# Optimization experiments

Hardware: AMD Instinct MI355X
Metric: run time of the kernel (lower is better)

Reference implementation:

```python
import jax, jax.numpy as jnp
from jax import lax
import numpy as np

EPS = 1e-5
K = 16
NUM_GROUP = 128
D = 384
HEADS = 6
DEPTH = 4
BETA = 0.25

def gelu(x):
    return jax.nn.gelu(x, approximate=False)

def linear(x, w, b):
    return x @ w.T + b

def layer_norm(x, g, b):
    mu = x.mean(-1, keepdims=True)
    var = x.var(-1, keepdims=True)
    return (x - mu) / jnp.sqrt(var + EPS) * g + b

def group_norm(x, gamma, beta, groups):
    B, C = x.shape[0], x.shape[1]
    sp = x.shape[2:]
    xg = x.reshape((B, groups, C // groups) + sp)
    axes = tuple(range(2, xg.ndim))
    mu = xg.mean(axes, keepdims=True)
    var = xg.var(axes, keepdims=True)
    xg = (xg - mu) / jnp.sqrt(var + EPS)
    x = xg.reshape((B, C) + sp)
    shp = (1, C) + (1,) * len(sp)
    return x * gamma.reshape(shp) + beta.reshape(shp)

def knn_idx(q, kp, k):
    # q [B,Nq,3], kp [B,Nk,3] -> idx [B,Nq,k] of k nearest keys
    d = jnp.sum(q * q, -1)[:, :, None] - 2.0 * jnp.einsum('bqd,bkd->bqk', q, kp) + jnp.sum(kp * kp, -1)[:, None, :]
    _, idx = lax.top_k(-d, k)
    return idx

def graph_feature(coor_q, x_q, coor_k, x_k, k):
    # coor [B,3,N], x [B,C,N] -> [B,2C,Nq,k]
    idx = knn_idx(coor_q.transpose(0, 2, 1), coor_k.transpose(0, 2, 1), k)
    feat = jax.vmap(lambda a, i: a[:, i])(x_k, idx)  # [B,C,Nq,k]
    xq = x_q[:, :, :, None]
    return jnp.concatenate([feat - xq, jnp.broadcast_to(xq, feat.shape)], axis=1)

def fps_indices(xyz, m):
    # farthest point sampling, start at index 0 (matches pointnet2)
    B, N, _ = xyz.shape
    def body(carry, _):
        dist, far = carry
        c = jnp.take_along_axis(xyz, far[:, None, None], axis=1)
        d = jnp.sum((xyz - c) ** 2, -1)
        dist = jnp.minimum(dist, d)
        return (dist, jnp.argmax(dist, -1).astype(jnp.int32)), far
    init = (jnp.full((B, N), 1e10, xyz.dtype), jnp.zeros((B,), jnp.int32))
    _, idxs = lax.scan(body, init, None, length=m)
    return idxs.T  # [B,m]

def gather_ch(x, idx):
    return jax.vmap(lambda a, i: a[:, i])(x, idx)

def conv1x1_2d(x, w):
    return jnp.einsum('oc,bcnk->bonk', w, x)

def conv1x1_1d(x, w, b):
    return jnp.einsum('oc,bcn->bon', w, x) + b[None, :, None]

def linear_resize(x, out_len):
    # F.interpolate(mode='linear', align_corners=False) along axis 1 of [B,N,D]
    n = x.shape[1]
    pos = (jnp.arange(out_len, dtype=x.dtype) + 0.5) * (n / out_len) - 0.5
    pos = jnp.clip(pos, 0.0, n - 1.0)
    i0 = jnp.floor(pos).astype(jnp.int32)
    i1 = jnp.minimum(i0 + 1, n - 1)
    w = (pos - i0.astype(x.dtype))[None, :, None]
    return x[:, i0] * (1.0 - w) + x[:, i1] * w

def vq(z, cb, beta):
    d = jnp.sum(z * z, -1, keepdims=True) - 2.0 * (z @ cb.T) + jnp.sum(cb * cb, -1)
    eidx = jnp.argmin(d, -1)
    q = cb[eidx]
    loss = jnp.mean((lax.stop_gradient(z) - q) ** 2) + beta * jnp.mean((z - lax.stop_gradient(q)) ** 2)
    q_st = z + lax.stop_gradient(q - z)  # straight-through
    return q_st, loss, eidx

def forward_core(xyz, it_w, it_b, g1_w, g1_g, g1_bt, g2_w, g2_g, g2_bt, g3_w, g3_g, g3_bt, g4_w, g4_g, g4_bt, pe_w1, pe_b1, pe_w2, pe_b2, ip_w1, ip_b1, ip_w2, ip_b2, ln1_g, ln1_b, qkv_w, qkv_b, o_w, o_b, ln2_g, ln2_b, m1_w, m1_b, m2_w, m2_b, pyr_w1, pyr_b1, pyr_g1, pyr_bt1, pyr_w2, pyr_b2, pyr_g2, pyr_bt2, fus_w, fus_b, cb0, cb1, cb2):
    B = xyz.shape[0]
    x = xyz.transpose(0, 2, 1)  # [B,7,N]
    coor, normal, plane = x[:, :3], x[:, 3:6], x[:, 6:7]
    f = conv1x1_1d(coor, it_w, it_b)  # [B,8,N]

    def edge_conv(cq, fq, ck, fk, w, g, bt, groups):
        h = graph_feature(cq, fq, ck, fk, K)
        h = conv1x1_2d(h, w)
        h = group_norm(h, g, bt, groups)
        h = jnp.where(h > 0, h, 0.2 * h)  # LeakyReLU(0.2)
        return h.max(axis=-1)

    f = edge_conv(coor, f, coor, f, g1_w, g1_g, g1_bt, 4)  # [B,32,N]
    idx = fps_indices(coor.transpose(0, 2, 1), NUM_GROUP)
    coor_q, normal_q, plane_q, f_q = gather_ch(coor, idx), gather_ch(normal, idx), gather_ch(plane, idx), gather_ch(f, idx)
    f = edge_conv(coor_q, f_q, coor, f, g2_w, g2_g, g2_bt, 4)  # [B,64,128]
    coor, normal, plane = coor_q, normal_q, plane_q
    f = edge_conv(coor, f, coor, f, g3_w, g3_g, g3_bt, 4)  # [B,64,128]
    idx = fps_indices(coor.transpose(0, 2, 1), NUM_GROUP)
    coor_q, normal_q, plane_q, f_q = gather_ch(coor, idx), gather_ch(normal, idx), gather_ch(plane, idx), gather_ch(f, idx)
    f = edge_conv(coor_q, f_q, coor, f, g4_w, g4_g, g4_bt, 4)  # [B,128,128]
    coor = coor_q.transpose(0, 2, 1)  # [B,128,3]
    f = f.transpose(0, 2, 1)          # [B,128,128]

    pe = linear(gelu(linear(coor, pe_w1, pe_b1)), pe_w2, pe_b2)
    h = linear(gelu(linear(f, ip_w1, ip_b1)), ip_w2, ip_b2)
    t = h + pe
    hd = D // HEADS
    scale = 1.0 / np.sqrt(hd)
    N = t.shape[1]
    for l in range(DEPTH):
        hn = layer_norm(t, ln1_g[l], ln1_b[l])
        qkv = hn @ qkv_w[l] + qkv_b[l]
        q, k_, v = jnp.split(qkv, 3, axis=-1)
        q = q.reshape(B, N, HEADS, hd)
        k_ = k_.reshape(B, N, HEADS, hd)
        v = v.reshape(B, N, HEADS, hd)
        att = jax.nn.softmax(jnp.einsum('bqhd,bkhd->bhqk', q, k_) * scale, axis=-1)
        o = jnp.einsum('bhqk,bkhd->bqhd', att, v).reshape(B, N, D)
        t = t + o @ o_w[l] + o_b[l]
        hn = layer_norm(t, ln2_g[l], ln2_b[l])
        t = t + gelu(hn @ m1_w[l] + m1_b[l]) @ m2_w[l] + m2_b[l]

    base = t  # [B,128,384]
    cbs = (cb0, cb1, cb2)
    outs, losses, idxs = [], [], []
    prev = None
    for level in range(3):
        res = max(base.shape[1] // (2 ** level), 8)
        if res == base.shape[1]:
            lf = base
        else:
            # adaptive_avg_pool1d with evenly dividing bins == reshape-mean
            lf = base.reshape(B, res, base.shape[1] // res, D).mean(2)
        c = lf.transpose(0, 2, 1)
        c = gelu(group_norm(conv1x1_1d(c, pyr_w1[level], pyr_b1[level]), pyr_g1[level], pyr_bt1[level], 8))
        c = gelu(group_norm(conv1x1_1d(c, pyr_w2[level], pyr_b2[level]), pyr_g2[level], pyr_bt2[level], 8))
        proc = c.transpose(0, 2, 1)
        if level > 0:
            pu = prev if prev.shape[1] == res else linear_resize(prev, res)
            proc = gelu(linear(jnp.concatenate([proc, pu], axis=-1), fus_w[level - 1], fus_b[level - 1]))
        q_st, loss, eidx = vq(proc, cbs[level], BETA)
        outs.append(q_st)
        losses.append(loss)
        idxs.append(eidx)
        prev = q_st
    return outs, losses, idxs

def setup_inputs():
    key = jax.random.key(0)
    cnt = [0]
    def nrm(shape, s=0.02):
        cnt[0] += 1
        return jax.random.normal(jax.random.fold_in(key, cnt[0]), shape, jnp.float32) * s
    L = 4
    inp = {}
    inp['xyz'] = nrm((8, 4096, 7), 1.0)
    inp['it_w'] = nrm((8, 3), 0.3)
    inp['it_b'] = jnp.zeros((8,), jnp.float32)
    inp['g1_w'] = nrm((32, 16), 0.1); inp['g1_g'] = jnp.ones((32,)); inp['g1_bt'] = jnp.zeros((32,))
    inp['g2_w'] = nrm((64, 64), 0.1); inp['g2_g'] = jnp.ones((64,)); inp['g2_bt'] = jnp.zeros((64,))
    inp['g3_w'] = nrm((64, 128), 0.1); inp['g3_g'] = jnp.ones((64,)); inp['g3_bt'] = jnp.zeros((64,))
    inp['g4_w'] = nrm((128, 128), 0.1); inp['g4_g'] = jnp.ones((128,)); inp['g4_bt'] = jnp.zeros((128,))
    inp['pe_w1'] = nrm((128, 3), 0.3); inp['pe_b1'] = jnp.zeros((128,))
    inp['pe_w2'] = nrm((D, 128), 0.05); inp['pe_b2'] = jnp.zeros((D,))
    inp['ip_w1'] = nrm((512, 128), 0.05); inp['ip_b1'] = jnp.zeros((512,))
    inp['ip_w2'] = nrm((D, 512), 0.03); inp['ip_b2'] = jnp.zeros((D,))
    inp['ln1_g'] = jnp.ones((L, D)); inp['ln1_b'] = jnp.zeros((L, D))
    inp['qkv_w'] = nrm((L, D, 3 * D)); inp['qkv_b'] = jnp.zeros((L, 3 * D))
    inp['o_w'] = nrm((L, D, D)); inp['o_b'] = jnp.zeros((L, D))
    inp['ln2_g'] = jnp.ones((L, D)); inp['ln2_b'] = jnp.zeros((L, D))
    inp['m1_w'] = nrm((L, D, 4 * D)); inp['m1_b'] = jnp.zeros((L, 4 * D))
    inp['m2_w'] = nrm((L, 4 * D, D)); inp['m2_b'] = jnp.zeros((L, D))
    inp['pyr_w1'] = nrm((3, 2 * D, D), 0.03); inp['pyr_b1'] = jnp.zeros((3, 2 * D))
    inp['pyr_g1'] = jnp.ones((3, 2 * D)); inp['pyr_bt1'] = jnp.zeros((3, 2 * D))
    inp['pyr_w2'] = nrm((3, D, 2 * D), 0.03); inp['pyr_b2'] = jnp.zeros((3, D))
    inp['pyr_g2'] = jnp.ones((3, D)); inp['pyr_bt2'] = jnp.zeros((3, D))
    inp['fus_w'] = nrm((2, D, 2 * D), 0.03); inp['fus_b'] = jnp.zeros((2, D))
    inp['cb0'] = nrm((8192, D), 0.5)
    inp['cb1'] = nrm((4096, D), 0.5)
    inp['cb2'] = nrm((2048, D), 0.5)
    return inp

def reference(xyz, it_w, it_b, g1_w, g1_g, g1_bt, g2_w, g2_g, g2_bt, g3_w, g3_g, g3_bt, g4_w, g4_g, g4_bt, pe_w1, pe_b1, pe_w2, pe_b2, ip_w1, ip_b1, ip_w2, ip_b2, ln1_g, ln1_b, qkv_w, qkv_b, o_w, o_b, ln2_g, ln2_b, m1_w, m1_b, m2_w, m2_b, pyr_w1, pyr_b1, pyr_g1, pyr_bt1, pyr_w2, pyr_b2, pyr_g2, pyr_bt2, fus_w, fus_b, cb0, cb1, cb2):
    outs, losses, idxs = forward_core(xyz, it_w, it_b, g1_w, g1_g, g1_bt, g2_w, g2_g, g2_bt, g3_w, g3_g, g3_bt, g4_w, g4_g, g4_bt, pe_w1, pe_b1, pe_w2, pe_b2, ip_w1, ip_b1, ip_w2, ip_b2, ln1_g, ln1_b, qkv_w, qkv_b, o_w, o_b, ln2_g, ln2_b, m1_w, m1_b, m2_w, m2_b, pyr_w1, pyr_b1, pyr_g1, pyr_bt1, pyr_w2, pyr_b2, pyr_g2, pyr_bt2, fus_w, fus_b, cb0, cb1, cb2)
    # concat quantized features of the 3 levels (128+64+32 tokens), total VQ loss, per-level indices
    return (jnp.concatenate(outs, axis=1), losses[0] + losses[1] + losses[2], idxs[0], idxs[1], idxs[2])
```

## Files before the change

### kernel.cpp

```cpp
#include <hip/hip_runtime.h>
#include <math.h>

#define EPSF 1e-5f

__device__ __forceinline__ float geluf(float x){
  return 0.5f*x*(1.0f + erff(x*0.70710678118654752440f));
}

typedef __attribute__((ext_vector_type(8))) short bf16x8;
typedef __attribute__((ext_vector_type(4))) float f32x4;

constexpr size_t WQKV = 0;
constexpr size_t WO   = WQKV + (size_t)4*1152*384;
constexpr size_t WM1  = WO   + (size_t)4*384*384;
constexpr size_t WM2  = WM1  + (size_t)4*1536*384;
constexpr size_t WIP1 = WM2  + (size_t)4*384*1536;
constexpr size_t WIP2 = WIP1 + (size_t)512*128;
constexpr size_t WPE2 = WIP2 + (size_t)384*512;
constexpr size_t WPY1 = WPE2 + (size_t)384*128;
constexpr size_t WPY2 = WPY1 + (size_t)3*768*384;
constexpr size_t WFUS = WPY2 + (size_t)3*384*768;
constexpr size_t WTOT = WFUS + (size_t)2*384*768;

__device__ __forceinline__ void split_rne(float x, short& h, short& l){
// ... 55 lines not shown
__global__ void gather_rows(const float* __restrict__ src, const int* __restrict__ idx,
                            float* __restrict__ dst, int B, int C, int N, int M){
  int i = blockIdx.x*blockDim.x + threadIdx.x;
  if(i >= B*M*C) return;
  int c = i % C; int m = (i/C)%M; int b = i/(C*M);
  dst[i] = src[((size_t)b*N + idx[b*M+m])*C + c];
}

__global__ void split_planes(const float* __restrict__ src, short* __restrict__ hi,
                             short* __restrict__ lo, int n4){
  int i = blockIdx.x*blockDim.x + threadIdx.x;
  if(i >= n4) return;
  split_quad(src + (size_t)i*4, (unsigned*)hi, (unsigned*)lo, i);
}

__global__ void split_cb3(const float* __restrict__ c0, const float* __restrict__ c1,
                          const float* __restrict__ c2, short* __restrict__ hi, short* __restrict__ lo){
  constexpr int N1 = 8192*384/4, N2 = 4096*384/4, N3 = 2048*384/4;
  int i = blockIdx.x*blockDim.x + threadIdx.x;
  if(i >= N1+N2+N3) return;
  const float* src; size_t q;
  if(i < N1){ src = c0; q = i; }
  else if(i < N1+N2){ src = c1; q = i - N1; }
  else { src = c2; q = i - N1 - N2; }
  split_quad(src + q*4, (unsigned*)hi, (unsigned*)lo, (size_t)i);
}

__global__ void cbsq3(const float* __restrict__ c0, const float* __restrict__ c1,
                      const float* __restrict__ c2, float* __restrict__ out){
  int c = blockIdx.x*blockDim.x + threadIdx.x;
  if(c >= 14336) return;
  const float* p;
  if(c < 8192) p = c0 + (size_t)c*384;
  else if(c < 12288) p = c1 + (size_t)(c-8192)*384;
  else p = c2 + (size_t)(c-12288)*384;
  float s=0.f;
  for(int d=0;d<384;d++) s = fmaf(p[d],p[d],s);
  out[c] = s;
}

__global__ void split_multi(const float* __restrict__ ip1, const float* __restrict__ ip2,
                            const float* __restrict__ pe2, const float* __restrict__ py1,
                            const float* __restrict__ py2, const float* __restrict__ fus,
                            short* __restrict__ hi, short* __restrict__ lo){
  constexpr int N1 = 512*128/4, N2 = 384*512/4, N3 = 384*128/4;
  constexpr int N4 = 3*768*384/4, N5 = 3*384*768/4, N6 = 2*384*768/4;
  int i = blockIdx.x*blockDim.x + threadIdx.x;
  const float* src; size_t q, dq;
  if(i < N1){ src=ip1; q=i; dq=WIP1/4+q; }
  else if(i < N1+N2){ src=ip2; q=i-N1; dq=WIP2/4+q; }
  else if(i < N1+N2+N3){ src=pe2; q=i-N1-N2; dq=WPE2/4+q; }
  else if(i < N1+N2+N3+N4){ src=py1; q=i-N1-N2-N3; dq=WPY1/4+q; }
  else if(i < N1+N2+N3+N4+N5){ src=py2; q=i-N1-N2-N3-N4; dq=WPY2/4+q; }
  else if(i < N1+N2+N3+N4+N5+N6){ src=fus; q=i-N1-N2-N3-N4-N5; dq=WFUS/4+q; }
  else return;
  split_quad(src + q*4, (unsigned*)hi, (unsigned*)lo, dq);
}

__global__ __launch_bounds__(256) void transpose_split(const float* __restrict__ src,
    short* __restrict__ hi, short* __restrict__ lo, int K, int N,
    size_t sstride, size_t dstride){
  __shared__ float tile[32][33];
  int l = blockIdx.z;
  src += (size_t)l*sstride; hi += (size_t)l*dstride; lo += (size_t)l*dstride;
  int bn = blockIdx.x*32, bk = blockIdx.y*32;
  int tx = threadIdx.x & 31, ty = threadIdx.x >> 5;
  #pragma unroll
  for(int i=ty; i<32; i+=8){
    int k = bk+i, n = bn+tx;
    tile[i][tx] = (k<K && n<N) ? src[(size_t)k*N+n] : 0.f;
  }
  __syncthreads();
  #pragma unroll
  for(int i=ty; i<32; i+=8){
    int n = bn+i, k = bk+tx;
    if(n<N && k<K){
      short h,l2; split_rne(tile[tx][i], h, l2);
      hi[(size_t)n*K+k] = h; lo[(size_t)n*K+k] = l2;
    }
  }
}

#define KNN_K 16
template<int NKMAX, int NT>
__global__ __launch_bounds__(NT) void knn2q_kernel(const float* __restrict__ Q, const float* __restrict__ Kp,
                                                   int* __restrict__ idxout, int B, int Nq, int Nk){
  constexpr int NW = NT/64;
  __shared__ float4 sk[NKMAX];
  __shared__ float scd[NW][2][64];
  __shared__ int   sci[NW][2][64];
  __shared__ int   scnt[NW][2];
  int qb = blockIdx.x*(NW*2);
  int b = qb / Nq;
  const float* kb = Kp + (size_t)b*3*Nk;
  if(threadIdx.x < NW*2) ((int*)scnt)[threadIdx.x] = 0;
  for(int n=threadIdx.x; n<Nk; n+=NT){
    float x = kb[n], y = kb[Nk+n], z = kb[2*Nk+n];
    sk[n] = make_float4(x, y, z, fmaf(x,x, fmaf(y,y, z*z)));
  }
  __syncthreads();
  int wave = threadIdx.x >> 6;
  int lane = threadIdx.x & 63;
  int nq0 = qb + wave*2 - b*Nq;
  float q0x = -2.0f*Q[((size_t)b*3+0)*Nq + nq0];
  float q0y = -2.0f*Q[((size_t)b*3+1)*Nq + nq0];
  float q0z = -2.0f*Q[((size_t)b*3+2)*Nq + nq0];
  float q1x = -2.0f*Q[((size_t)b*3+0)*Nq + nq0+1];
  float q1y = -2.0f*Q[((size_t)b*3+1)*Nq + nq0+1];
  float q1z = -2.0f*Q[((size_t)b*3+2)*Nq + nq0+1];

  float mind0 = INFINITY, mind1 = INFINITY;
  for(int n=lane; n<Nk; n+=64){
    float4 k4 = sk[n];
    float d0 = fmaf(q0x, k4.x, fmaf(q0y, k4.y, fmaf(q0z, k4.z, k4.w)));
    float d1 = fmaf(q1x, k4.x, fmaf(q1y, k4.y, fmaf(q1z, k4.z, k4.w)));
    mind0 = fminf(mind0, d0);
    mind1 = fminf(mind1, d1);
  }
  {
    float v0 = mind0, v1 = mind1;
    #pragma unroll
    for(int k=2;k<=64;k<<=1){
      #pragma unroll
      for(int j=k>>1;j>=1;j>>=1){
        float o0 = __shfl_xor(v0, j, 64);
        float o1 = __shfl_xor(v1, j, 64);
        bool keepmin = ((lane & j)==0) == ((lane & k)==0);
        v0 = keepmin ? fminf(v0,o0) : fmaxf(v0,o0);
        v1 = keepmin ? fminf(v1,o1) : fmaxf(v1,o1);
      }
    }
    mind0 = v0; mind1 = v1;
  }
  float tau0 = __shfl(mind0, 15, 64);
  float tau1 = __shfl(mind1, 15, 64);

  for(int n=lane; n<Nk; n+=64){
    float4 k4 = sk[n];
    float d0 = fmaf(q0x, k4.x, fmaf(q0y, k4.y, fmaf(q0z, k4.z, k4.w)));
    float d1 = fmaf(q1x, k4.x, fmaf(q1y, k4.y, fmaf(q1z, k4.z, k4.w)));
    if(d0 <= tau0){
      int slot = atomicAdd(&scnt[wave][0], 1);
      if(slot < 64){ scd[wave][0][slot] = d0; sci[wave][0][slot] = n; }
    }
    if(d1 <= tau1){
      int slot = atomicAdd(&scnt[wave][1], 1);
      if(slot < 64){ scd[wave][1][slot] = d1; sci[wave][1][slot] = n; }
    }
  }
  __syncthreads();

  #pragma unroll
  for(int qq=0; qq<2; qq++){
    int cnt = scnt[wave][qq];
    int* orow = idxout + ((size_t)b*Nq + nq0 + qq)*KNN_K;
    float nqx = qq ? q1x : q0x;
    float nqy = qq ? q1y : q0y;
    float nqz = qq ? q1z : q0z;
    if(cnt <= 64){
      float d = (lane < cnt) ? scd[wave][qq][lane] : INFINITY;
      int  id = (lane < cnt) ? sci[wave][qq][lane] : 0x7fffffff;
      #pragma unroll
      for(int k=2;k<=64;k<<=1){
        #pragma unroll
        for(int j=k>>1;j>=1;j>>=1){
          float od = __shfl_xor(d, j, 64);
          int oi = __shfl_xor(id, j, 64);
          bool lower = (lane & j)==0;
          bool asc = (lane & k)==0;
          bool otherSmaller = (od < d) || (od==d && oi < id);
          if((lower==asc) == otherSmaller){ d = od; id = oi; }
        }
      }
      if(lane < KNN_K) orow[lane] = id;
    } else {
      float bd[KNN_K]; int bi2[KNN_K];
      #pragma unroll
      for(int j=0;j<KNN_K;j++){ bd[j]=INFINITY; bi2[j]=0x7fffffff; }
      float curmax = INFINITY;
      for(int n=lane; n<Nk; n+=64){
        float4 k4 = sk[n];
        float d = fmaf(nqx, k4.x, fmaf(nqy, k4.y, fmaf(nqz, k4.z, k4.w)));
        if(d < curmax){
          int pm = 0; float md = bd[0]; int mi = bi2[0];
          #pragma unroll
          for(int j=1;j<KNN_K;j++){
            if(bd[j] > md || (bd[j]==md && bi2[j] > mi)){ md=bd[j]; mi=bi2[j]; pm=j; }
          }
          #pragma unroll
          for(int j=0;j<KNN_K;j++){ if(j==pm){ bd[j]=d; bi2[j]=n; } }
          float m2 = -INFINITY;
          #pragma unroll
          for(int j=0;j<KNN_K;j++) m2 = fmaxf(m2, bd[j]);
          curmax = m2;
        }
      }
      for(int t=0;t<KNN_K;t++){
        float ld = bd[0]; int li_ = bi2[0];
        #pragma unroll
        for(int j=1;j<KNN_K;j++){
          if(bd[j] < ld || (bd[j]==ld && bi2[j] < li_)){ ld=bd[j]; li_=bi2[j]; }
        }
        float wd = ld; int wi = li_;
        #pragma unroll
        for(int m=1;m<64;m<<=1){
          float od = __shfl_xor(wd, m, 64);
          int oi = __shfl_xor(wi, m, 64);
          if(od < wd || (od==wd && oi < wi)){ wd=od; wi=oi; }
        }
        if(ld==wd && li_==wi){
          #pragma unroll
          for(int j=0;j<KNN_K;j++){ if(bd[j]==wd && bi2[j]==wi){ bd[j]=INFINITY; bi2[j]=0x7fffffff; } }
        }
        if(lane==0) orow[t] = wi;
      }
    }
  }
}

template<int NMAX, int PPT, int NT>
__global__ __launch_bounds__(NT) void fps_kernel(const float* __restrict__ coor, int* __restrict__ out,
                                                 int N, int M){
  __shared__ float skx[NMAX], sky[NMAX], skz[NMAX];
  __shared__ unsigned long long swk[2][NT/64];
  constexpr int NW = NT/64;
  int b = blockIdx.x;
  int tid = threadIdx.x;
  int lane = tid & 63, wid = tid >> 6;
  const float* cx = coor + (size_t)b*3*N;
  const float* cy = cx + N;
  const float* cz = cx + 2*N;
  float px[PPT], py[PPT], pz[PPT], dist[PPT];
  #pragma unroll
  for(int j=0;j<PPT;j++){
    int n = tid + j*NT;
    float x = cx[n], y = cy[n], z = cz[n];
    px[j]=x; py[j]=y; pz[j]=z; dist[j]=1e10f;
    skx[n]=x; sky[n]=y; skz[n]=z;
  }
  if(tid==0) out[b*M] = 0;
  __syncthreads();
  float fx = skx[0], fy = sky[0], fz = skz[0];
  for(int t=1;t<M;t++){
    unsigned long long bk = 0ull;
    #pragma unroll
    for(int j=0;j<PPT;j++){
      int n = tid + j*NT;
      float dx = __fsub_rn(px[j], fx);
      float dy = __fsub_rn(py[j], fy);
      float dz = __fsub_rn(pz[j], fz);
      float d = __fadd_rn(__fadd_rn(__fmul_rn(dx,dx), __fmul_rn(dy,dy)), __fmul_rn(dz,dz));
      float nd = fminf(dist[j], d);
      dist[j] = nd;
      union{float f; unsigned u;} db; db.f = nd;
      unsigned long long key = ((unsigned long long)db.u << 32) | (unsigned)(0x7fffffff - n);
      bk = (key > bk) ? key : bk;
    }
    #pragma unroll
// ... 494 lines not shown

  int ar_ = t >> 2, akq = (t & 3)*16;
  bf16x8 pah[2], pal[2], pbh[2], pbl[2];
  auto loadT = [&](int k0){
    const short* hp = Ahi + (size_t)(bm + ar_)*K + k0 + akq;
    const short* lp = Alo + (size_t)(bm + ar_)*K + k0 + akq;
    pah[0] = *(const bf16x8*)hp; pah[1] = *(const bf16x8*)(hp+8);
    pal[0] = *(const bf16x8*)lp; pal[1] = *(const bf16x8*)(lp+8);
    const short* hq = Bhi + (size_t)(bn + ar_)*K + k0 + akq;
    const short* lq = Blo + (size_t)(bn + ar_)*K + k0 + akq;
    pbh[0] = *(const bf16x8*)hq; pbh[1] = *(const bf16x8*)(hq+8);
    pbl[0] = *(const bf16x8*)lq; pbl[1] = *(const bf16x8*)(lq+8);
  };
  auto stageT = [&](){
    *(bf16x8*)&sAhi[ar_][akq]   = pah[0];
    *(bf16x8*)&sAhi[ar_][akq+8] = pah[1];
    *(bf16x8*)&sAlo[ar_][akq]   = pal[0];
    *(bf16x8*)&sAlo[ar_][akq+8] = pal[1];
    *(bf16x8*)&sBhi[ar_][akq]   = pbh[0];
    *(bf16x8*)&sBhi[ar_][akq+8] = pbh[1];
    *(bf16x8*)&sBlo[ar_][akq]   = pbl[0];
    *(bf16x8*)&sBlo[ar_][akq+8] = pbl[1];
  };

  loadT(0);
  int nk = K >> 6;
  for(int ki=0; ki<nk; ki++){
    stageT();
    __syncthreads();
    if(ki+1 < nk) loadT((ki+1)*64);
    #pragma unroll
    for(int half=0; half<2; half++){
      bf16x8 ah[2], al[2], bh[2], bl[2];
      #pragma unroll
      for(int m=0;m<2;m++){
        int arow = wm*32 + m*16 + rr;
        ah[m] = *(bf16x8*)&sAhi[arow][half*32 + g*8];
        al[m] = *(bf16x8*)&sAlo[arow][half*32 + g*8];
      }
      #pragma unroll
      for(int n=0;n<2;n++){
        int bcol = wn*32 + n*16 + rr;
        bh[n] = *(bf16x8*)&sBhi[bcol][half*32 + g*8];
        bl[n] = *(bf16x8*)&sBlo[bcol][half*32 + g*8];
      }
      #pragma unroll
      for(int m=0;m<2;m++){
        #pragma unroll
        for(int n=0;n<2;n++){
          acc[m][n] = __builtin_amdgcn_mfma_f32_16x16x32_bf16(ah[m], bh[n], acc[m][n], 0, 0, 0);
          acc[m][n] = __builtin_amdgcn_mfma_f32_16x16x32_bf16(ah[m], bl[n], acc[m][n], 0, 0, 0);
          acc[m][n] = __builtin_amdgcn_mfma_f32_16x16x32_bf16(al[m], bh[n], acc[m][n], 0, 0, 0);
        }
      }
    }
    __syncthreads();
  }
  #pragma unroll
  for(int m=0;m<2;m++){
    #pragma unroll
    for(int r4=0;r4<4;r4++){
      int row = bm + wm*32 + m*16 + g*4 + r4;
      unsigned long long kmin = 0xFFFFFFFFFFFFFFFFull;
      #pragma unroll
      for(int n=0;n<2;n++){
        int col = bn + wn*32 + n*16 + rr;
        float v = cbsq[col] - 2.0f*acc[m][n][r4];
        union{float f; unsigned u;} vb; vb.f = v;
        unsigned s = (unsigned)((int)vb.u >> 31);
        unsigned mapped = vb.u ^ (s | 0x80000000u);
        unsigned long long key = ((unsigned long long)mapped << 32) | (unsigned)col;
        kmin = key < kmin ? key : kmin;
      }
      #pragma unroll
      for(int msk=1; msk<16; msk<<=1){
        unsigned long long o = __shfl_xor(kmin, msk, 64);
        kmin = o < kmin ? o : kmin;
      }
      if(rr == 0) atomicMin(&keys[row], kmin);
    }
  }
}

__global__ __launch_bounds__(128) void attn_kernel(const float* __restrict__ qkv, float* __restrict__ out){
  int bh = blockIdx.x; int b = bh/6, h = bh%6;
  __shared__ float sk[128][64]; __shared__ float sv[128][64];
  const float* base = qkv + (size_t)b*128*1152;
  for(int i=threadIdx.x;i<128*64;i+=128){
    int n = i>>6, d = i&63;
    sk[n][d] = base[(size_t)n*1152 + 384 + h*64 + d];
    sv[n][d] = base[(size_t)n*1152 + 768 + h*64 + d];
  }
  __syncthreads();
  int n = threadIdx.x;
  float q[64];
  #pragma unroll
  for(int d=0;d<64;d++) q[d] = base[(size_t)n*1152 + h*64 + d];
  float m = -INFINITY, Z = 0.f;
  float acc[64];
  #pragma unroll
  for(int d=0;d<64;d++) acc[d]=0.f;
  for(int j=0;j<128;j++){
    float s=0.f;
    #pragma unroll
    for(int d=0;d<64;d++) s = fmaf(q[d], sk[j][d], s);
    s *= 0.125f;
    if(s > m){
      float sc = expf(m - s);
      Z *= sc;
      #pragma unroll
      for(int d=0;d<64;d++) acc[d] *= sc;
      m = s;
    }
    float e = expf(s - m);
    Z += e;
    #pragma unroll
    for(int d=0;d<64;d++) acc[d] = fmaf(e, sv[j][d], acc[d]);
  }
  float invZ = 1.0f/Z;
  float* outp = out + ((size_t)b*128 + n)*384 + h*64;
  #pragma unroll
  for(int d=0;d<64;d++) outp[d] = acc[d]*invZ;
}

__global__ __launch_bounds__(256) void gn_gelu_kernel(float* __restrict__ x, const float* __restrict__ gamma,
                                                      const float* __restrict__ beta, int res, int C, int Cg){
  int b = blockIdx.x / 8; int gr = blockIdx.x % 8;
  int total = res*Cg;
  float s=0.f, q=0.f;
  for(int i=threadIdx.x;i<total;i+=256){
    int n = i/Cg, c = gr*Cg + i%Cg;
    float v = x[((size_t)b*res+n)*C + c];
    s += v; q += v*v;
  }
  __shared__ float rs[256], rq[256];
  rs[threadIdx.x]=s; rq[threadIdx.x]=q; __syncthreads();
  for(int st=128;st>0;st>>=1){
    if(threadIdx.x<st){ rs[threadIdx.x]+=rs[threadIdx.x+st]; rq[threadIdx.x]+=rq[threadIdx.x+st]; }
    __syncthreads();
  }
  float mean = rs[0]/(float)total;
  float var = rq[0]/(float)total - mean*mean; var = fmaxf(var, 0.f);
  float rstd = 1.0f/sqrtf(var+EPSF);
  __syncthreads();
  for(int i=threadIdx.x;i<total;i+=256){
    int n = i/Cg, c = gr*Cg + i%Cg;
    size_t off = ((size_t)b*res+n)*C + c;
    float hn = (x[off]-mean)*rstd*gamma[c] + beta[c];
    x[off] = geluf(hn);
  }
}

__global__ void pool_kernel(const float* __restrict__ t, float* __restrict__ lf, int B, int res, int r){
  int i = blockIdx.x*blockDim.x + threadIdx.x;
  if(i >= B*res*384) return;
  int c = i%384; int n = (i/384)%res; int b = i/(384*res);
  const float* tp = t + ((size_t)b*(res*r) + n*r)*384 + c;
  float v;
  if(r==2) v = (tp[0] + tp[384])*0.5f;
  else     v = ((tp[0]+tp[384]) + (tp[2*384]+tp[3*384]))*0.25f;
  lf[i] = v;
}

__global__ void pu_cat_kernel(const float* __restrict__ proc, const float* __restrict__ outbuf,
                              float* __restrict__ cat, int B, int res, int prevoff){
  int i = blockIdx.x*blockDim.x + threadIdx.x;
  if(i >= B*res*768) return;
  int c = i%768; int n = (i/768)%res; int b = i/(768*res);
  float v;
  if(c < 384) v = proc[((size_t)b*res+n)*384 + c];
  else {
    int cc = c-384;
    const float* p0 = outbuf + ((size_t)b*224 + prevoff + 2*n)*384 + cc;
    v = p0[0]*0.5f + p0[384]*0.5f;
  }
  cat[i] = v;
}

__global__ __launch_bounds__(128) void vq_out_kernel(const float* __restrict__ z,
    const unsigned long long* __restrict__ keys,
    const float* __restrict__ cb, float* __restrict__ out, float* __restrict__ lossacc,
    int res, int rowoff, float* __restrict__ idxout){
  int row = blockIdx.x;
  int b = row/res, n = row%res;
  int e = (int)(unsigned)(keys[row] & 0xffffffffull);
  const float* zr = z + (size_t)row*384;
  const float* q = cb + (size_t)e*384;
  float* o = out + ((size_t)b*224 + rowoff + n)*384;
  float ls = 0.f;
  for(int d=threadIdx.x; d<384; d+=128){
    float zd = zr[d], qd = q[d];
    o[d] = zd + (qd - zd);
    float df = zd - qd;
    ls = fmaf(df,df,ls);
  }
  __shared__ float red[128];
  red[threadIdx.x]=ls; __syncthreads();
  for(int st=64;st>0;st>>=1){ if(threadIdx.x<st) red[threadIdx.x]+=red[threadIdx.x+st]; __syncthreads(); }
  if(threadIdx.x==0){
    atomicAdd(lossacc, red[0]);
    idxout[row] = (float)e;
  }
}

__global__ void loss_kernel(const float* __restrict__ lossacc, float* __restrict__ out){
// ... 108 lines not shown
  float* f1    = ws + OFF_F1;
  int*   idx1  = (int*)(ws + OFF_IDX1);
  int*   fps1  = (int*)(ws + OFF_FPS1);
  float* coor1 = ws + OFF_COOR1;
  float* f1q   = ws + OFF_F1Q;
  int*   idx2  = (int*)(ws + OFF_IDX2);
  float* f2    = ws + OFF_F2;
  int*   idx3  = (int*)(ws + OFF_IDX3);
  float* f3    = ws + OFF_F3;
  int*   fps2  = (int*)(ws + OFF_FPS2);
  float* coor2 = ws + OFF_COOR2;
  float* f3q   = ws + OFF_F3Q;
  int*   idx4  = (int*)(ws + OFF_IDX4);
  float* f4    = ws + OFF_F4;
  float* coorT = ws + OFF_COORT;
  float* tmp   = ws + OFF_TMP;
  float* tbuf  = ws + OFF_T;
  float* qkvb  = ws + OFF_QKV;
  float* attb  = ws + OFF_ATT;
  float* midb  = ws + OFF_MID;
  float* lfb   = ws + OFF_LF;
  float* c1b   = ws + OFF_C1;
  float* c2b   = ws + OFF_C2;
  float* catb  = ws + OFF_CAT;
  float* procb = ws + OFF_PROC;
  unsigned long long* keys = (unsigned long long*)(ws + OFF_KEYS);
  float* cbsq  = ws + OFF_CBSQ;
  float* part  = ws + OFF_PART;
  float* mr    = ws + OFF_MR;
  float* lossa = ws + OFF_LOSS;
  short* zhi   = (short*)(ws + OFF_ZHI);
  short* zlo   = (short*)(ws + OFF_ZLO);
  short* cbhi  = (short*)(ws + OFF_CBHI);
  short* cblo  = (short*)(ws + OFF_CBLO);
  short* whi   = (short*)(ws + OFF_WHI);
  short* wlo   = (short*)(ws + OFF_WLO);

  bool presplit = ws_size >= OFF_END * sizeof(float);

  auto cdiv = [](int a, int b){ return (a+b-1)/b; };
  auto gemm_full = [&](const float* A, const float* Bm, const float* bias, float* C,
                       int M, int N, int K, int BT, int act, int addto,
                       const float* lng, const float* lnb){
    if(((K & 63) == 0) && ((N & 63) == 0) && ((M & 63) == 0)){
      dim3 g(N/64, M/64);
      gemm_mfma<<<g, 256, 0, stream>>>(A, Bm, bias, C, M, N, K, BT, act, addto, lng, lnb);
    } else {
      dim3 g(N/64, M/64), blk(128);
      gemm64<<<g, blk, 0, stream>>>(A, Bm, bias, C, M, N, K, BT, act, addto);
    }
  };
  auto gemmW = [&](const float* A, const float* W, size_t wofs, const float* bias, float* C,
                   int M, int N, int K, int BT, int act, int addto,
                   const float* lng, const float* lnb){
    if(presplit && ((K & 63) == 0) && ((N & 63) == 0) && ((M & 63) == 0)){
      dim3 g(N/64, M/64);
      gemm_mfma_ps<<<g, 256, 0, stream>>>(A, whi + wofs, wlo + wofs, bias, C, M, N, K, act, addto, lng, lnb);
    } else {
      gemm_full(A, W, bias, C, M, N, K, BT, act, addto, lng, lnb);
    }
  };

  hipMemsetAsync(lossa, 0, 8*sizeof(float), stream);
  hipMemsetAsync(keys, 0xFF, 1792*sizeof(unsigned long long), stream);

  init_pts<<<cdiv(B_*N0,256),256,0,stream>>>(xyz, it_w, it_b, coor0, f0, B_, N0);

  split_cb3<<<cdiv(14336*384/4,256),256,0,stream>>>(cb0, cb1, cb2, cbhi, cblo);
  cbsq3<<<cdiv(14336,256),256,0,stream>>>(cb0, cb1, cb2, cbsq);

  if(presplit){
    transpose_split<<<dim3(1152/32,384/32,4),256,0,stream>>>(qkv_w, whi+WQKV, wlo+WQKV, 384, 1152,
        (size_t)384*1152, (size_t)1152*384);
    transpose_split<<<dim3(384/32,384/32,4),256,0,stream>>>(o_w, whi+WO, wlo+WO, 384, 384,
        (size_t)384*384, (size_t)384*384);
    transpose_split<<<dim3(1536/32,384/32,4),256,0,stream>>>(m1_w, whi+WM1, wlo+WM1, 384, 1536,
        (size_t)384*1536, (size_t)1536*384);
    transpose_split<<<dim3(384/32,1536/32,4),256,0,stream>>>(m2_w, whi+WM2, wlo+WM2, 1536, 384,
        (size_t)1536*384, (size_t)384*1536);
    int totq = (512*128 + 384*512 + 384*128 + 3*768*384 + 3*384*768 + 2*384*768)/4;
    split_multi<<<cdiv(totq,256),256,0,stream>>>(ip_w1, ip_w2, pe_w2, pyr_w1, pyr_w2, fus_w, whi, wlo);
  }

  knn2q_kernel<4096,512><<<B_*N0/16,512,0,stream>>>(coor0, coor0, idx1, B_, N0, N0);
  ec_main<8,32><<<B_*32*N0/256,256,0,stream>>>(f0, f0, idx1, g1_w, f1, part, N0, N0);
  ec_reduce<<<32,256,0,stream>>>(part, mr, 32*N0/256, 1.0f/(8.0f*N0*16.0f));
  ec_norm<<<cdiv(B_*32*N0,256),256,0,stream>>>(f1, mr, g1_g, g1_bt, N0, 32, B_*32*N0);

  fps_kernel<4096,8,512><<<B_,512,0,stream>>>(coor0, fps1, N0, M0);
  gather_ch_kernel<<<cdiv(B_*3*M0,256),256,0,stream>>>(coor0, fps1, coor1, B_, 3, N0, M0);
  gather_rows<<<cdiv(B_*M0*32,256),256,0,stream>>>(f1, fps1, f1q, B_, 32, N0, M0);

  knn2q_kernel<4096,512><<<B_*M0/16,512,0,stream>>>(coor1, coor0, idx2, B_, M0, N0);
  ec_main<32,64><<<B_*64*M0/256,256,0,stream>>>(f1q, f1, idx2, g2_w, f2, part, M0, N0);
  ec_reduce<<<32,256,0,stream>>>(part, mr, 64*M0/256, 1.0f/(16.0f*M0*16.0f));
  ec_norm<<<cdiv(B_*64*M0,256),256,0,stream>>>(f2, mr, g2_g, g2_bt, M0, 64, B_*64*M0);

  knn2q_kernel<128,512><<<B_*M0/16,512,0,stream>>>(coor1, coor1, idx3, B_, M0, M0);
  ec_main<64,64><<<B_*64*M0/256,256,0,stream>>>(f2, f2, idx3, g3_w, f3, part, M0, M0);
  ec_reduce<<<32,256,0,stream>>>(part, mr, 64*M0/256, 1.0f/(16.0f*M0*16.0f));
  ec_norm<<<cdiv(B_*64*M0,256),256,0,stream>>>(f3, mr, g3_g, g3_bt, M0, 64, B_*64*M0);

  fps_kernel<128,1,128><<<B_,128,0,stream>>>(coor1, fps2, M0, M0);
  gather_ch_kernel<<<cdiv(B_*3*M0,256),256,0,stream>>>(coor1, fps2, coor2, B_, 3, M0, M0);
  gather_rows<<<cdiv(B_*M0*64,256),256,0,stream>>>(f3, fps2, f3q, B_, 64, M0, M0);

  knn2q_kernel<128,512><<<B_*M0/16,512,0,stream>>>(coor2, coor1, idx4, B_, M0, M0);
  ec_main<64,128><<<B_*128*M0/256,256,0,stream>>>(f3q, f3, idx4, g4_w, f4, part, M0, M0);
  ec_reduce<<<32,256,0,stream>>>(part, mr, 128*M0/256, 1.0f/(32.0f*M0*16.0f));
  ec_norm<<<cdiv(B_*128*M0,256),256,0,stream>>>(f4, mr, g4_g, g4_bt, M0, 128, B_*128*M0);

  transpose_cn<<<cdiv(B_*3*M0,256),256,0,stream>>>(coor2, coorT, B_, 3, M0);

  gemm_full(coorT, pe_w1, pe_b1, tmp, 1024, 128, 3, 1, 1, 0, nullptr, nullptr);
  gemmW(tmp, pe_w2, WPE2, pe_b2, tbuf, 1024, 384, 128, 1, 0, 0, nullptr, nullptr);
  gemmW(f4, ip_w1, WIP1, ip_b1, tmp, 1024, 512, 128, 1, 1, 0, nullptr, nullptr);
  gemmW(tmp, ip_w2, WIP2, ip_b2, tbuf, 1024, 384, 512, 1, 0, 1, nullptr, nullptr);

  for(int l=0;l<4;l++){
    gemmW(tbuf, qkv_w + (size_t)l*384*1152, WQKV + (size_t)l*1152*384, qkv_b + l*1152, qkvb,
          1024, 1152, 384, 0, 0, 0, ln1_g + l*384, ln1_b + l*384);
    attn_kernel<<<48,128,0,stream>>>(qkvb, attb);
    gemmW(attb, o_w + (size_t)l*384*384, WO + (size_t)l*384*384, o_b + l*384, tbuf,
          1024, 384, 384, 0, 0, 1, nullptr, nullptr);
    gemmW(tbuf, m1_w + (size_t)l*384*1536, WM1 + (size_t)l*1536*384, m1_b + l*1536, midb,
          1024, 1536, 384, 0, 1, 0, ln2_g + l*384, ln2_b + l*384);
    gemmW(midb, m2_w + (size_t)l*1536*384, WM2 + (size_t)l*384*1536, m2_b + l*384, tbuf,
          1024, 384, 1536, 0, 0, 1, nullptr, nullptr);
  }

  const float* cbs[3] = {cb0, cb1, cb2};
  const int ncodes[3] = {8192, 4096, 2048};
  const int cboff[3]  = {0, 8192, 12288};
  const int keyoff[3] = {0, 1024, 1536};
  const int rowoffs[3] = {0, 128, 192};
  const size_t OUT0 = (size_t)8*224*384;
  float* idxouts[3] = { out + OUT0 + 1, out + OUT0 + 1 + 1024, out + OUT0 + 1 + 1536 };

  for(int lv=0; lv<3; ++lv){
    int res = 128 >> lv;
    int rows = 8*res;
    const float* lf;
    if(lv==0){ lf = tbuf; }
    else {
      pool_kernel<<<cdiv(rows*384,256),256,0,stream>>>(tbuf, lfb, B_, res, 1<<lv);
      lf = lfb;
    }
    gemmW(lf, pyr_w1 + (size_t)lv*768*384, WPY1 + (size_t)lv*768*384, pyr_b1 + lv*768, c1b,
          rows, 768, 384, 1, 0, 0, nullptr, nullptr);
    gn_gelu_kernel<<<64,256,0,stream>>>(c1b, pyr_g1 + lv*768, pyr_bt1 + lv*768, res, 768, 96);
    gemmW(c1b, pyr_w2 + (size_t)lv*384*768, WPY2 + (size_t)lv*384*768, pyr_b2 + lv*384, c2b,
          rows, 384, 768, 1, 0, 0, nullptr, nullptr);
    gn_gelu_kernel<<<64,256,0,stream>>>(c2b, pyr_g2 + lv*384, pyr_bt2 + lv*384, res, 384, 48);
    const float* z = c2b;
    if(lv > 0){
      pu_cat_kernel<<<cdiv(rows*768,256),256,0,stream>>>(c2b, out, catb, B_, res, rowoffs[lv-1]);
      gemmW(catb, fus_w + (size_t)(lv-1)*384*768, WFUS + (size_t)(lv-1)*384*768, fus_b + (lv-1)*384, procb,
            rows, 384, 768, 1, 1, 0, nullptr, nullptr);
      z = procb;
    }
    split_planes<<<cdiv(rows*384/4,256),256,0,stream>>>(z, zhi, zlo, rows*384/4);
    gemm_vq<<<dim3(ncodes[lv]/64, rows/64), 256, 0, stream>>>(zhi, zlo,
        cbhi + (size_t)cboff[lv]*384, cblo + (size_t)cboff[lv]*384,
        cbsq + cboff[lv], keys + keyoff[lv], rows, ncodes[lv], 384);
    vq_out_kernel<<<rows,128,0,stream>>>(z, keys + keyoff[lv], cbs[lv], out, lossa + lv, res,
                                         rowoffs[lv], idxouts[lv]);
  }

  loss_kernel<<<1,1,0,stream>>>(lossa, out + OUT0);
}
```

Before: 1.621 ms.

## Process four kNN queries per wave and split attention head dim across lanes

The kNN kernel now handles four queries per wave instead of two, which halves the grid and amortizes the shared-memory key loads across more queries; candidate slots shrink to 48 per query to fit LDS. The attention kernel splits each query's 64-wide head dimension across four lane groups and reduces the partial scores with shuffles. This quadruples threads per block and reduces per-thread register arrays, raising parallelism in a kernel that previously launched only 48 blocks of 128 threads. Fewer candidate slots make the slow fallback path more likely when distance ties exceed 48, and the kNN change also raises register pressure.

Result: faster. 1.474 ms (-9.1%).

```diff
diff --git a/kernel.cpp b/kernel.cpp
--- a/kernel.cpp
+++ b/kernel.cpp
@@ -161,18 +161,19 @@
 }
 
 #define KNN_K 16
+#define KNN_SLOTS 48
 template<int NKMAX, int NT>
-__global__ __launch_bounds__(NT) void knn2q_kernel(const float* __restrict__ Q, const float* __restrict__ Kp,
+__global__ __launch_bounds__(NT) void knn4q_kernel(const float* __restrict__ Q, const float* __restrict__ Kp,
                                                    int* __restrict__ idxout, int B, int Nq, int Nk){
   constexpr int NW = NT/64;
   __shared__ float4 sk[NKMAX];
-  __shared__ float scd[NW][2][64];
-  __shared__ int   sci[NW][2][64];
-  __shared__ int   scnt[NW][2];
-  int qb = blockIdx.x*(NW*2);
+  __shared__ float scd[NW][4][KNN_SLOTS];
+  __shared__ int   sci[NW][4][KNN_SLOTS];
+  __shared__ int   scnt[NW][4];
+  int qb = blockIdx.x*(NW*4);
   int b = qb / Nq;
   const float* kb = Kp + (size_t)b*3*Nk;
-  if(threadIdx.x < NW*2) ((int*)scnt)[threadIdx.x] = 0;
+  if(threadIdx.x < NW*4) ((int*)scnt)[threadIdx.x] = 0;
   for(int n=threadIdx.x; n<Nk; n+=NT){
     float x = kb[n], y = kb[Nk+n], z = kb[2*Nk+n];
     sk[n] = make_float4(x, y, z, fmaf(x,x, fmaf(y,y, z*z)));
@@ -180,63 +181,65 @@
   __syncthreads();
   int wave = threadIdx.x >> 6;
   int lane = threadIdx.x & 63;
-  int nq0 = qb + wave*2 - b*Nq;
-  float q0x = -2.0f*Q[((size_t)b*3+0)*Nq + nq0];
-  float q0y = -2.0f*Q[((size_t)b*3+1)*Nq + nq0];
-  float q0z = -2.0f*Q[((size_t)b*3+2)*Nq + nq0];
-  float q1x = -2.0f*Q[((size_t)b*3+0)*Nq + nq0+1];
-  float q1y = -2.0f*Q[((size_t)b*3+1)*Nq + nq0+1];
-  float q1z = -2.0f*Q[((size_t)b*3+2)*Nq + nq0+1];
-
-  float mind0 = INFINITY, mind1 = INFINITY;
+  int nq0 = qb + wave*4 - b*Nq;
+  float qx[4], qy[4], qz[4];
+  #pragma unroll
+  for(int qq=0;qq<4;qq++){
+    qx[qq] = -2.0f*Q[((size_t)b*3+0)*Nq + nq0+qq];
+    qy[qq] = -2.0f*Q[((size_t)b*3+1)*Nq + nq0+qq];
+    qz[qq] = -2.0f*Q[((size_t)b*3+2)*Nq + nq0+qq];
+  }
+
+  float mind[4] = {INFINITY, INFINITY, INFINITY, INFINITY};
   for(int n=lane; n<Nk; n+=64){
     float4 k4 = sk[n];
-    float d0 = fmaf(q0x, k4.x, fmaf(q0y, k4.y, fmaf(q0z, k4.z, k4.w)));
-    float d1 = fmaf(q1x, k4.x, fmaf(q1y, k4.y, fmaf(q1z, k4.z, k4.w)));
-    mind0 = fminf(mind0, d0);
-    mind1 = fminf(mind1, d1);
+    #pragma unroll
+    for(int qq=0;qq<4;qq++){
+      float d = fmaf(qx[qq], k4.x, fmaf(qy[qq], k4.y, fmaf(qz[qq], k4.z, k4.w)));
+      mind[qq] = fminf(mind[qq], d);
+    }
   }
   {
-    float v0 = mind0, v1 = mind1;
+    float v0=mind[0], v1=mind[1], v2=mind[2], v3=mind[3];
     #pragma unroll
     for(int k=2;k<=64;k<<=1){
       #pragma unroll
       for(int j=k>>1;j>=1;j>>=1){
         float o0 = __shfl_xor(v0, j, 64);
         float o1 = __shfl_xor(v1, j, 64);
+        float o2 = __shfl_xor(v2, j, 64);
+        float o3 = __shfl_xor(v3, j, 64);
         bool keepmin = ((lane & j)==0) == ((lane & k)==0);
         v0 = keepmin ? fminf(v0,o0) : fmaxf(v0,o0);
         v1 = keepmin ? fminf(v1,o1) : fmaxf(v1,o1);
-      }
-    }
-    mind0 = v0; mind1 = v1;
-  }
-  float tau0 = __shfl(mind0, 15, 64);
-  float tau1 = __shfl(mind1, 15, 64);
+        v2 = keepmin ? fminf(v2,o2) : fmaxf(v2,o2);
+        v3 = keepmin ? fminf(v3,o3) : fmaxf(v3,o3);
+      }
+    }
+    mind[0]=v0; mind[1]=v1; mind[2]=v2; mind[3]=v3;
+  }
+  float tau[4];
+  #pragma unroll
+  for(int qq=0;qq<4;qq++) tau[qq] = __shfl(mind[qq], 15, 64);
 
   for(int n=lane; n<Nk; n+=64){
     float4 k4 = sk[n];
-    float d0 = fmaf(q0x, k4.x, fmaf(q0y, k4.y, fmaf(q0z, k4.z, k4.w)));
-    float d1 = fmaf(q1x, k4.x, fmaf(q1y, k4.y, fmaf(q1z, k4.z, k4.w)));
-    if(d0 <= tau0){
-      int slot = atomicAdd(&scnt[wave][0], 1);
-      if(slot < 64){ scd[wave][0][slot] = d0; sci[wave][0][slot] = n; }
-    }
-    if(d1 <= tau1){
-      int slot = atomicAdd(&scnt[wave][1], 1);
-      if(slot < 64){ scd[wave][1][slot] = d1; sci[wave][1][slot] = n; }
+    #pragma unroll
+    for(int qq=0;qq<4;qq++){
+      float d = fmaf(qx[qq], k4.x, fmaf(qy[qq], k4.y, fmaf(qz[qq], k4.z, k4.w)));
+      if(d <= tau[qq]){
+        int slot = atomicAdd(&scnt[wave][qq], 1);
+        if(slot < KNN_SLOTS){ scd[wave][qq][slot] = d; sci[wave][qq][slot] = n; }
+      }
     }
   }
   __syncthreads();
 
   #pragma unroll
-  for(int qq=0; qq<2; qq++){
+  for(int qq=0; qq<4; qq++){
     int cnt = scnt[wave][qq];
     int* orow = idxout + ((size_t)b*Nq + nq0 + qq)*KNN_K;
-    float nqx = qq ? q1x : q0x;
-    float nqy = qq ? q1y : q0y;
-    float nqz = qq ? q1z : q0z;
-    if(cnt <= 64){
+    if(cnt <= KNN_SLOTS){
       float d = (lane < cnt) ? scd[wave][qq][lane] : INFINITY;
       int  id = (lane < cnt) ? sci[wave][qq][lane] : 0x7fffffff;
       #pragma unroll
@@ -253,6 +256,7 @@
       }
       if(lane < KNN_K) orow[lane] = id;
     } else {
+      float nqx = qx[qq], nqy = qy[qq], nqz = qz[qq];
       float bd[KNN_K]; int bi2[KNN_K];
       #pragma unroll
       for(int j=0;j<KNN_K;j++){ bd[j]=INFINITY; bi2[j]=0x7fffffff; }
@@ -913,45 +917,51 @@
   }
 }
 
-__global__ __launch_bounds__(128) void attn_kernel(const float* __restrict__ qkv, float* __restrict__ out){
+__global__ __launch_bounds__(512) void attn_kernel(const float* __restrict__ qkv, float* __restrict__ out){
   int bh = blockIdx.x; int b = bh/6, h = bh%6;
   __shared__ float sk[128][64]; __shared__ float sv[128][64];
   const float* base = qkv + (size_t)b*128*1152;
-  for(int i=threadIdx.x;i<128*64;i+=128){
+  for(int i=threadIdx.x;i<128*64;i+=512){
     int n = i>>6, d = i&63;
     sk[n][d] = base[(size_t)n*1152 + 384 + h*64 + d];
     sv[n][d] = base[(size_t)n*1152 + 768 + h*64 + d];
   }
   __syncthreads();
-  int n = threadIdx.x;
-  float q[64];
-  #pragma unroll
-  for(int d=0;d<64;d++) q[d] = base[(size_t)n*1152 + h*64 + d];
+  int wave = threadIdx.x >> 6;
+  int lane = threadIdx.x & 63;
+  int part = lane >> 4;
+  int n = wave*16 + (lane & 15);
+  int d0 = part*16;
+  float q[16];
+  #pragma unroll
+  for(int d=0;d<16;d++) q[d] = base[(size_t)n*1152 + h*64 + d0 + d];
   float m = -INFINITY, Z = 0.f;
-  float acc[64];
-  #pragma unroll
-  for(int d=0;d<64;d++) acc[d]=0.f;
+  float acc[16];
+  #pragma unroll
+  for(int d=0;d<16;d++) acc[d]=0.f;
   for(int j=0;j<128;j++){
-    float s=0.f;
-    #pragma unroll
-    for(int d=0;d<64;d++) s = fmaf(q[d], sk[j][d], s);
+    float sp = 0.f;
+    #pragma unroll
+    for(int d=0;d<16;d++) sp = fmaf(q[d], sk[j][d0 + d], sp);
+    float s = sp + __shfl_xor(sp, 16, 64);
+    s = s + __shfl_xor(s, 32, 64);
     s *= 0.125f;
     if(s > m){
       float sc = expf(m - s);
       Z *= sc;
       #pragma unroll
-      for(int d=0;d<64;d++) acc[d] *= sc;
+      for(int d=0;d<16;d++) acc[d] *= sc;
       m = s;
     }
     float e = expf(s - m);
     Z += e;
     #pragma unroll
-    for(int d=0;d<64;d++) acc[d] = fmaf(e, sv[j][d], acc[d]);
+    for(int d=0;d<16;d++) acc[d] = fmaf(e, sv[j][d0 + d], acc[d]);
   }
   float invZ = 1.0f/Z;
-  float* outp = out + ((size_t)b*128 + n)*384 + h*64;
-  #pragma unroll
-  for(int d=0;d<64;d++) outp[d] = acc[d]*invZ;
+  float* outp = out + ((size_t)b*128 + n)*384 + h*64 + d0;
+  #pragma unroll
+  for(int d=0;d<16;d++) outp[d] = acc[d]*invZ;
 }
 
 __global__ __launch_bounds__(256) void gn_gelu_kernel(float* __restrict__ x, const float* __restrict__ gamma,
@@ -1226,7 +1236,7 @@
     split_multi<<<cdiv(totq,256),256,0,stream>>>(ip_w1, ip_w2, pe_w2, pyr_w1, pyr_w2, fus_w, whi, wlo);
   }
 
-  knn2q_kernel<4096,512><<<B_*N0/16,512,0,stream>>>(coor0, coor0, idx1, B_, N0, N0);
+  knn4q_kernel<4096,512><<<B_*N0/32,512,0,stream>>>(coor0, coor0, idx1, B_, N0, N0);
   ec_main<8,32><<<B_*32*N0/256,256,0,stream>>>(f0, f0, idx1, g1_w, f1, part, N0, N0);
   ec_reduce<<<32,256,0,stream>>>(part, mr, 32*N0/256, 1.0f/(8.0f*N0*16.0f));
   ec_norm<<<cdiv(B_*32*N0,256),256,0,stream>>>(f1, mr, g1_g, g1_bt, N0, 32, B_*32*N0);
@@ -1235,12 +1245,12 @@
   gather_ch_kernel<<<cdiv(B_*3*M0,256),256,0,stream>>>(coor0, fps1, coor1, B_, 3, N0, M0);
   gather_rows<<<cdiv(B_*M0*32,256),256,0,stream>>>(f1, fps1, f1q, B_, 32, N0, M0);
 
-  knn2q_kernel<4096,512><<<B_*M0/16,512,0,stream>>>(coor1, coor0, idx2, B_, M0, N0);
+  knn4q_kernel<4096,512><<<B_*M0/32,512,0,stream>>>(coor1, coor0, idx2, B_, M0, N0);
   ec_main<32,64><<<B_*64*M0/256,256,0,stream>>>(f1q, f1, idx2, g2_w, f2, part, M0, N0);
   ec_reduce<<<32,256,0,stream>>>(part, mr, 64*M0/256, 1.0f/(16.0f*M0*16.0f));
   ec_norm<<<cdiv(B_*64*M0,256),256,0,stream>>>(f2, mr, g2_g, g2_bt, M0, 64, B_*64*M0);
 
-  knn2q_kernel<128,512><<<B_*M0/16,512,0,stream>>>(coor1, coor1, idx3, B_, M0, M0);
+  knn4q_kernel<128,512><<<B_*M0/32,512,0,stream>>>(coor1, coor1, idx3, B_, M0, M0);
   ec_main<64,64><<<B_*64*M0/256,256,0,stream>>>(f2, f2, idx3, g3_w, f3, part, M0, M0);
   ec_reduce<<<32,256,0,stream>>>(part, mr, 64*M0/256, 1.0f/(16.0f*M0*16.0f));
   ec_norm<<<cdiv(B_*64*M0,256),256,0,stream>>>(f3, mr, g3_g, g3_bt, M0, 64, B_*64*M0);
@@ -1249,7 +1259,7 @@
   gather_ch_kernel<<<cdiv(B_*3*M0,256),256,0,stream>>>(coor1, fps2, coor2, B_, 3, M0, M0);
   gather_rows<<<cdiv(B_*M0*64,256),256,0,stream>>>(f3, fps2, f3q, B_, 64, M0, M0);
 
-  knn2q_kernel<128,512><<<B_*M0/16,512,0,stream>>>(coor2, coor1, idx4, B_, M0, M0);
+  knn4q_kernel<128,512><<<B_*M0/32,512,0,stream>>>(coor2, coor1, idx4, B_, M0, M0);
   ec_main<64,128><<<B_*128*M0/256,256,0,stream>>>(f3q, f3, idx4, g4_w, f4, part, M0, M0);
   ec_reduce<<<32,256,0,stream>>>(part, mr, 128*M0/256, 1.0f/(32.0f*M0*16.0f));
   ec_norm<<<cdiv(B_*128*M0,256),256,0,stream>>>(f4, mr, g4_g, g4_bt, M0, 128, B_*128*M0);
@@ -1264,7 +1274,7 @@
   for(int l=0;l<4;l++){
     gemmW(tbuf, qkv_w + (size_t)l*384*1152, WQKV + (size_t)l*1152*384, qkv_b + l*1152, qkvb,
           1024, 1152, 384, 0, 0, 0, ln1_g + l*384, ln1_b + l*384);
-    attn_kernel<<<48,128,0,stream>>>(qkvb, attb);
+    attn_kernel<<<48,512,0,stream>>>(qkvb, attb);
     gemmW(attb, o_w + (size_t)l*384*384, WO + (size_t)l*384*384, o_b + l*384, tbuf,
           1024, 384, 384, 0, 0, 1, nullptr, nullptr);
     gemmW(tbuf, m1_w + (size_t)l*384*1536, WM1 + (size_t)l*1536*384, m1_b + l*1536, midb,
```
